# Optimization experiments

Hardware: AMD Instinct MI355X
Metric: run time of the kernel (lower is better)

The kernel has to match this reference:

```python
import jax, jax.numpy as jnp
import numpy as np

N = 50000      # nodes per graph side
E = 800000     # edges per graph side
G = 128        # number of graphs in the batch
D = 256        # input feature dim
L = 1024       # number of output labels
NEG_SLOPE = 0.2


def _gat_layer(x, src, dst, W, a_src, a_dst, b, n_nodes):
    """Single-head GATConv with self-loops already included in (src, dst)."""
    h = x @ W                                   # [N, F]
    s_src = h @ a_src                           # [N] per-node source score
    s_dst = h @ a_dst                           # [N] per-node dest score
    e = jax.nn.leaky_relu(s_src[src] + s_dst[dst], NEG_SLOPE)   # [E']
    m = jax.ops.segment_max(e, dst, num_segments=n_nodes)        # segment softmax (stable)
    ex = jnp.exp(e - m[dst])
    denom = jax.ops.segment_sum(ex, dst, num_segments=n_nodes)
    alpha = ex / denom[dst]                     # [E']
    out = jax.ops.segment_sum(h[src] * alpha[:, None], dst, num_segments=n_nodes)
    return out + b


def _mean_pool(x, batch, n_graphs):
    s = jax.ops.segment_sum(x, batch, num_segments=n_graphs)
    cnt = jax.ops.segment_sum(jnp.ones((x.shape[0],), x.dtype), batch, num_segments=n_graphs)
    return s / jnp.maximum(cnt, 1.0)[:, None]


def setup_inputs() -> dict:
    key = jax.random.key(0)
    ks = jax.random.split(key, 24)
    p = lambda k, shape: (jax.random.normal(k, shape, jnp.float32) * 0.05)
    inp = {
        "x_s": jax.random.normal(ks[0], (N, D), jnp.float32),
        "x_t": jax.random.normal(ks[1], (N, D), jnp.float32),
        "edge_index_s": jax.random.randint(ks[2], (2, E), 0, N, jnp.int32),
        "edge_index_t": jax.random.randint(ks[3], (2, E), 0, N, jnp.int32),
        "xs_batch": jnp.sort(jax.random.randint(ks[4], (N,), 0, G, jnp.int32)),
        "xt_batch": jnp.sort(jax.random.randint(ks[5], (N,), 0, G, jnp.int32)),
        # source-graph GAT layers: 256->128, 128->64
        "Ws1": p(ks[6], (D, D // 2)), "as1_src": p(ks[7], (D // 2,)), "as1_dst": p(ks[8], (D // 2,)), "bs1": jnp.zeros((D // 2,), jnp.float32),
        "Ws2": p(ks[9], (D // 2, D // 4)), "as2_src": p(ks[10], (D // 4,)), "as2_dst": p(ks[11], (D // 4,)), "bs2": jnp.zeros((D // 4,), jnp.float32),
        # target-graph GAT layers
        "Wt1": p(ks[12], (D, D // 2)), "at1_src": p(ks[13], (D // 2,)), "at1_dst": p(ks[14], (D // 2,)), "bt1": jnp.zeros((D // 2,), jnp.float32),
        "Wt2": p(ks[15], (D // 2, D // 4)), "at2_src": p(ks[16], (D // 4,)), "at2_dst": p(ks[17], (D // 4,)), "bt2": jnp.zeros((D // 4,), jnp.float32),
        # classifier head
        "Wlin": p(ks[18], (D // 4, L)), "blin": jnp.zeros((L,), jnp.float32),
    }
    return inp


def reference(x_s, x_t, edge_index_s, edge_index_t, xs_batch, xt_batch,
              Ws1, as1_src, as1_dst, bs1, Ws2, as2_src, as2_dst, bs2,
              Wt1, at1_src, at1_dst, bt1, Wt2, at2_src, at2_dst, bt2,
              Wlin, blin):
    loop = jnp.arange(N, dtype=edge_index_s.dtype)
    src_s = jnp.concatenate([edge_index_s[0], loop])   # add self-loops (PyG default)
    dst_s = jnp.concatenate([edge_index_s[1], loop])
    src_t = jnp.concatenate([edge_index_t[0], loop])
    dst_t = jnp.concatenate([edge_index_t[1], loop])

    x1 = jax.nn.relu(_gat_layer(x_s, src_s, dst_s, Ws1, as1_src, as1_dst, bs1, N))
    x2 = jax.nn.relu(_gat_layer(x1, src_s, dst_s, Ws2, as2_src, as2_dst, bs2, N))
    xs = _mean_pool(x2, xs_batch, G)                   # [G, 64]

    x3 = jax.nn.relu(_gat_layer(x_t, src_t, dst_t, Wt1, at1_src, at1_dst, bt1, N))
    x4 = jax.nn.relu(_gat_layer(x3, src_t, dst_t, Wt2, at2_src, at2_dst, bt2, N))
    xt = _mean_pool(x4, xt_batch, G)                   # [G, 64]

    out = (xs + xt) @ Wlin + blin                      # [G, L]
    return jax.nn.sigmoid(out)
```

## Files before the change

kernel.cpp:

```cpp
#include <hip/hip_runtime.h>
#include <hip/hip_bf16.h>
#include <math.h>

constexpr int Nn   = 50000;
constexpr int Ecnt = 800000;
constexpr int Gn   = 128;
constexpr int Din  = 256;
constexpr int Lout = 1024;

constexpr int BKT_SH = 7;
constexpr int NBKT   = (Nn + 127) >> BKT_SH;
constexpr int CHUNK  = 4096;
constexpr int EBC    = (Ecnt + CHUNK - 1) / CHUNK;
constexpr size_t HS  = (size_t)Nn * 64;

typedef __attribute__((ext_vector_type(8))) short short8;
typedef __attribute__((ext_vector_type(4))) float f32x4;
typedef __attribute__((ext_vector_type(2))) float v2f;

__device__ __forceinline__ float lrelu(float x) { return x >= 0.f ? x : 0.2f * x; }

__device__ __forceinline__ float bflo(uint32_t v) { return __uint_as_float(v << 16); }
__device__ __forceinline__ float bfhi(uint32_t v) { return __uint_as_float(v & 0xffff0000u); }
__device__ __forceinline__ uint32_t f2bf(float f) {
    uint32_t x = __float_as_uint(f);
    return (x + 0x7fffu + ((x >> 16) & 1u)) >> 16;
}
__device__ __forceinline__ uint32_t packbf(float lo, float hi) {
    return f2bf(lo) | (f2bf(hi) << 16);
}

__global__ __launch_bounds__(512) void bkt_scan2(const int* __restrict__ bkt_cnt_b,
                                                 int* __restrict__ bkt_ptr_b,
                                                 int* __restrict__ bkt_cur_b,
                                                 int* __restrict__ row_ptr_b) {
    int side = blockIdx.x;
    const int* bkt_cnt = bkt_cnt_b + (size_t)side * (NBKT + 1);
    int* bkt_ptr = bkt_ptr_b + (size_t)side * (NBKT + 1);
    int* bkt_cur = bkt_cur_b + (size_t)side * (NBKT + 1);
    int* row_ptr = row_ptr_b + (size_t)side * (Nn + 1);
    __shared__ int buf[512];
    int t = threadIdx.x;
    int v = (t < NBKT) ? bkt_cnt[t] : 0;
    buf[t] = v;
    __syncthreads();
    for (int off = 1; off < 512; off <<= 1) {
        int x = (t >= off) ? buf[t - off] : 0;
        __syncthreads();
        buf[t] += x;
        __syncthreads();
    }
    if (t < NBKT) {
        int excl = buf[t] - v;
        bkt_ptr[t] = excl;
        bkt_cur[t] = excl;
    }
    if (t == 511) {
        bkt_ptr[NBKT] = buf[511];
        row_ptr[Nn]   = buf[511];
    }
}

__global__ __launch_bounds__(256) void bkt_scatter2(const int* __restrict__ e0,
                                                    const int* __restrict__ e1,
                                                    int* __restrict__ bkt_cur_b,
                                                    uint32_t* __restrict__ bkt_edges_b, int E) {
    int side = blockIdx.y;
    const int* src = side ? e1 : e0;
    const int* dst = src + E;
    int* bkt_cur = bkt_cur_b + (size_t)side * (NBKT + 1);
    uint32_t* bkt_edges = bkt_edges_b + (size_t)side * Ecnt;
    __shared__ int h[NBKT];
    __shared__ int cur[NBKT];
    for (int i = threadIdx.x; i < NBKT; i += 256) h[i] = 0;
    __syncthreads();
    int base = blockIdx.x * CHUNK;
    int end = min(base + CHUNK, E);
    for (int i = base + threadIdx.x; i < end; i += 256)
        atomicAdd(&h[dst[i] >> BKT_SH], 1);
    __syncthreads();
    for (int i = threadIdx.x; i < NBKT; i += 256) {
        int c = h[i];
        h[i] = c ? atomicAdd(&bkt_cur[i], c) : 0;
        cur[i] = 0;
    }
    __syncthreads();
    for (int i = base + threadIdx.x; i < end; i += 256) {
        int d = dst[i], b = d >> BKT_SH;
        int pos = h[b] + atomicAdd(&cur[b], 1);
        bkt_edges[pos] = (uint32_t)src[i] | ((uint32_t)(d & 127) << 16);
    }
}

__global__ __launch_bounds__(256) void csr_finalize2(const uint32_t* __restrict__ bkt_edges_b,
                                                     const int* __restrict__ bkt_ptr_b,
                                                     int* __restrict__ row_ptr_b,
                                                     int* __restrict__ csr_b, int n) {
    int side = blockIdx.y;
    const uint32_t* bkt_edges = bkt_edges_b + (size_t)side * Ecnt;
    const int* bkt_ptr = bkt_ptr_b + (size_t)side * (NBKT + 1);
    int* row_ptr = row_ptr_b + (size_t)side * (Nn + 1);
    int* csr = csr_b + (size_t)side * Ecnt;
    int b = blockIdx.x;
    int base = bkt_ptr[b];
    int cnt  = bkt_ptr[b + 1] - base;
    __shared__ int hist[128], curs[128], sc[128];
    int t = threadIdx.x;
    if (t < 128) hist[t] = 0;
    __syncthreads();
    for (int i = t; i < cnt; i += 256)
        atomicAdd(&hist[(bkt_edges[base + i] >> 16) & 127], 1);
    __syncthreads();
    if (t < 128) sc[t] = hist[t];
    __syncthreads();
    for (int off = 1; off < 128; off <<= 1) {
        int x = (t >= off && t < 128) ? sc[t - off] : 0;
        __syncthreads();
        if (t < 128) sc[t] += x;
        __syncthreads();
    }
    if (t < 128) {
        int excl = sc[t] - hist[t];
        int node = (b << BKT_SH) + t;
        if (node < n) row_ptr[node] = base + excl;
        curs[t] = excl;
    }
    __syncthreads();
    for (int i = t; i < cnt; i += 256) {
        uint32_t e = bkt_edges[base + i];
        int pos = atomicAdd(&curs[(e >> 16) & 127], 1);
        csr[base + pos] = (int)(e & 0xFFFFu);
    }
}

template<int MF, int NF, int BN, bool BF16A, bool FUSE_COUNT>
__global__ __launch_bounds__(256) void mfma_gemm2(
        const void* __restrict__ A0, const void* __restrict__ A1,
        const float* __restrict__ B0, const float* __restrict__ B1,
        uint32_t* __restrict__ Cb, size_t cstride,
        const float* __restrict__ as0, const float* __restrict__ as1,
        const float* __restrict__ ad0, const float* __restrict__ ad1,
        float* __restrict__ ssrc_b, float* __restrict__ sdst_b,
        int M, int K,
        const int* __restrict__ e0, const int* __restrict__ e1,
        int* __restrict__ bkt_cnt_b) {
    __shared__ uint32_t Al[64][36];
    __shared__ uint32_t Bl[BN][36];
    __shared__ float sS[64][2], sD[64][2];
    int side = blockIdx.y;

    if constexpr (FUSE_COUNT) {
        int gb = (M + 63) >> 6;
        if ((int)blockIdx.x >= gb) {
            int chunk = blockIdx.x - gb;
            const int* dst = (side ? e1 : e0) + Ecnt;
            int* bkt_cnt = bkt_cnt_b + (size_t)side * (NBKT + 1);
            int* hh = (int*)&Al[0][0];
            for (int i = threadIdx.x; i < NBKT; i += 256) hh[i] = 0;
            __syncthreads();
            int base = chunk * CHUNK;
            int end = min(base + CHUNK, Ecnt);
            for (int i = base + threadIdx.x; i < end; i += 256)
                atomicAdd(&hh[dst[i] >> BKT_SH], 1);
            __syncthreads();
            for (int i = threadIdx.x; i < NBKT; i += 256) {
                int c = hh[i];
                if (c) atomicAdd(&bkt_cnt[i], c);
            }
            return;
        }
    }

    const void* Av = side ? A1 : A0;
    const float* B = side ? B1 : B0;
    const float* Asrc = side ? as1 : as0;
    const float* Adst = side ? ad1 : ad0;
    uint32_t* C = Cb + (size_t)side * cstride;
    float* ssrc = ssrc_b + (size_t)side * Nn;
    float* sdst = sdst_b + (size_t)side * Nn;

    int tid  = threadIdx.x;
    int lane = tid & 63;
    int wid  = tid >> 6;
    int wr = wid >> 1, wc = wid & 1;
    int bm = blockIdx.x * 64;

    int arow = tid >> 2, aq = tid & 3;
    bool avalid = (bm + arow) < M;
    constexpr int NPI = BN * 16 / 256;

    float    fA[16];
    uint32_t uA[8];
    float    fB[NPI][4];

    auto LOADA = [&](int k0) {
        if constexpr (BF16A) {
            const uint32_t* A = (const uint32_t*)Av;
            if (avalid) {
                const uint32_t* p = A + (size_t)(bm + arow) * (K >> 1) + (k0 >> 1) + aq * 8;
                uint4 u0 = *(const uint4*)p;
                uint4 u1 = *(const uint4*)(p + 4);
                uA[0] = u0.x; uA[1] = u0.y; uA[2] = u0.z; uA[3] = u0.w;
                uA[4] = u1.x; uA[5] = u1.y; uA[6] = u1.z; uA[7] = u1.w;
            } else {
                #pragma unroll
                for (int i = 0; i < 8; i++) uA[i] = 0u;
            }
        } else {
            const float* A = (const float*)Av;
            if (avalid) {
                const float* p = A + (size_t)(bm + arow) * K + k0 + aq * 16;
                #pragma unroll
                for (int i = 0; i < 4; i++) {
                    float4 f = *(const float4*)(p + i * 4);
                    fA[4 * i] = f.x; fA[4 * i + 1] = f.y; fA[4 * i + 2] = f.z; fA[4 * i + 3] = f.w;
                }
            } else {
                #pragma unroll
                for (int i = 0; i < 16; i++) fA[i] = 0.f;
            }
        }
    };
    auto LOADB = [&](int k0) {
        #pragma unroll
        for (int it = 0; it < NPI; it++) {
            int pi = tid + it * 256;
            int n = pi & (BN - 1);
            int kp = pi / BN;
            const float* p = B + (size_t)(k0 + 4 * kp) * BN + n;
            fB[it][0] = p[0];
            fB[it][1] = p[BN];
            fB[it][2] = p[2 * BN];
            fB[it][3] = p[3 * BN];
        }
    };
    auto WRITE = [&]() {
        if constexpr (BF16A) {
            uint4* dst = (uint4*)&Al[arow][aq * 8];
            dst[0] = make_uint4(uA[0], uA[1], uA[2], uA[3]);
            dst[1] = make_uint4(uA[4], uA[5], uA[6], uA[7]);
        } else {
            uint32_t d[8];
            #pragma unroll
            for (int i = 0; i < 8; i++) d[i] = packbf(fA[2 * i], fA[2 * i + 1]);
            uint4* dst = (uint4*)&Al[arow][aq * 8];
            dst[0] = make_uint4(d[0], d[1], d[2], d[3]);
            dst[1] = make_uint4(d[4], d[5], d[6], d[7]);
        }
        #pragma unroll
        for (int it = 0; it < NPI; it++) {
            int pi = tid + it * 256;
            int n = pi & (BN - 1);
            int kp = pi / BN;
            *(uint2*)&Bl[n][2 * kp] = make_uint2(packbf(fB[it][0], fB[it][1]),
                                                 packbf(fB[it][2], fB[it][3]));
        }
    };

    f32x4 acc[MF][NF];
    #pragma unroll
    for (int i = 0; i < MF; i++)
        #pragma unroll
        for (int j = 0; j < NF; j++) acc[i][j] = (f32x4){0.f, 0.f, 0.f, 0.f};

    LOADA(0); LOADB(0);
    const int T = K / 64;
    for (int t = 0; t < T; t++) {
        WRITE();
        __syncthreads();
        if (t + 1 < T) { LOADA((t + 1) * 64); LOADB((t + 1) * 64); }
        int lr = lane & 15, lk = lane >> 4;
        #pragma unroll
        for (int ks = 0; ks < 2; ks++) {
            short8 af[MF], bf[NF];
            #pragma unroll
            for (int mf = 0; mf < MF; mf++)
                af[mf] = *(const short8*)&Al[wr * (MF * 16) + mf * 16 + lr][ks * 16 + lk * 4];
            #pragma unroll
            for (int nf = 0; nf < NF; nf++)
                bf[nf] = *(const short8*)&Bl[wc * (NF * 16) + nf * 16 + lr][ks * 16 + lk * 4];
            #pragma unroll
            for (int mf = 0; mf < MF; mf++)
                #pragma unroll
                for (int nf = 0; nf < NF; nf++)
                    acc[mf][nf] = __builtin_amdgcn_mfma_f32_16x16x32_bf16(af[mf], bf[nf], acc[mf][nf], 0, 0, 0);
        }
        __syncthreads();
    }

    int lr = lane & 15, lg = lane >> 4;
    {
        float a_s[NF], a_d[NF];
        #pragma unroll
        for (int nf = 0; nf < NF; nf++) {
            int col = wc * (NF * 16) + nf * 16 + lr;
            a_s[nf] = Asrc[col];
            a_d[nf] = Adst[col];
        }
        #pragma unroll
        for (int mf = 0; mf < MF; mf++) {
            #pragma unroll
            for (int j = 0; j < 4; j++) {
                float ps = 0.f, pd = 0.f;
                #pragma unroll
                for (int nf = 0; nf < NF; nf++) {
                    float v = acc[mf][nf][j];
                    ps += v * a_s[nf];
                    pd += v * a_d[nf];
                }
                #pragma unroll
                for (int o = 1; o < 16; o <<= 1) {
                    ps += __shfl_xor(ps, o);
                    pd += __shfl_xor(pd, o);
                }
                if (lr == 0) {
                    int rl = wr * (MF * 16) + mf * 16 + lg * 4 + j;
                    sS[rl][wc] = ps;
                    sD[rl][wc] = pd;
                }
            }
        }
    }
    #pragma unroll
    for (int mf = 0; mf < MF; mf++) {
        #pragma unroll
        for (int nf = 0; nf < NF; nf++) {
            int col = wc * (NF * 16) + nf * 16 + lr;
            #pragma unroll
            for (int j = 0; j < 4; j++) {
                int row = bm + wr * (MF * 16) + mf * 16 + lg * 4 + j;
                float v = acc[mf][nf][j];
                float w1 = __shfl_xor(v, 1);
                uint32_t p01 = (uint32_t)__builtin_amdgcn_cvt_pk_fp8_f32(v, w1, 0, false);
                uint32_t p23 = __shfl_xor(p01, 2);
                if (((lane & 3) == 0) && row < M)
                    C[(size_t)row * (BN >> 2) + (col >> 2)] = (p01 & 0xffffu) | (p23 << 16);
            }
        }
    }
    __syncthreads();
    if (tid < 64) {
        int row = bm + tid;
        if (row < M) {
            ssrc[row] = sS[tid][0] + sS[tid][1];
            sdst[row] = sD[tid][0] + sD[tid][1];
        }
    }
}

template<int F>
__global__ __launch_bounds__(256) void attn_agg2(const uint32_t* __restrict__ hb,
        const float* __restrict__ ssrc_b, const float* __restrict__ sdst_b,
        const int* __restrict__ row_ptr_b, const int* __restrict__ csr_b,
        const float* __restrict__ bias0, const float* __restrict__ bias1,
        uint32_t* __restrict__ xout_b, int n) {
    constexpr size_t HSTR = (size_t)Nn * (F / 4);
    constexpr int HD = F / 4;
    constexpr int XD = F / 2;
    int side = blockIdx.y;
    const uint32_t* h = hb + (size_t)side * HSTR;
    const float* ssrc = ssrc_b + (size_t)side * Nn;
    const float* sdst = sdst_b + (size_t)side * Nn;
    const int* row_ptr = row_ptr_b + (size_t)side * (Nn + 1);
    const int* csr_src = csr_b + (size_t)side * Ecnt;
    const float* bias = side ? bias1 : bias0;
    uint32_t* xout = xout_b + (size_t)side * HS;

    int wave = (blockIdx.x * blockDim.x + threadIdx.x) >> 6;
    int lane = threadIdx.x & 63;
    int half = lane >> 5;
    int lane5 = lane & 31;
    int wid = wave * 2 + half;
    if (wid >= n) return;
    int beg = row_ptr[wid], end = row_ptr[wid + 1];
    int deg = end - beg;
    float sd = sdst[wid];
    float eself = lrelu(ssrc[wid] + sd);
    int base32 = lane & 32;

    v2f a0 = {0.f, 0.f}, a1 = {0.f, 0.f}, a2 = {0.f, 0.f}, a3 = {0.f, 0.f};
    auto FMA8 = [&](uint2 u, float wj) {
        v2f p0 = __builtin_amdgcn_cvt_pk_f32_fp8(u.x, false);
        v2f p1 = __builtin_amdgcn_cvt_pk_f32_fp8(u.x, true);
        v2f p2 = __builtin_amdgcn_cvt_pk_f32_fp8(u.y, false);
        v2f p3 = __builtin_amdgcn_cvt_pk_f32_fp8(u.y, true);
        v2f wv = {wj, wj};
        a0 += p0 * wv; a1 += p1 * wv; a2 += p2 * wv; a3 += p3 * wv;
    };

    if (deg <= 32) {
        int p = beg + lane5;
        bool act = lane5 < deg;
        int s = act ? csr_src[p] : 0;
        float e = act ? lrelu(ssrc[s] + sd) : -1e30f;
        float m = fmaxf(eself, e);
        #pragma unroll
        for (int o = 16; o; o >>= 1) m = fmaxf(m, __shfl_xor(m, o));
        float ex = act ? __expf(e - m) : 0.f;
        float dsum = ex;
        #pragma unroll
        for (int o = 16; o; o >>= 1) dsum += __shfl_xor(dsum, o);
        float exself = __expf(eself - m);
        dsum += exself;
        float inv = 1.f / dsum;
        float w = ex * inv;
        float wself = exself * inv;

        if constexpr (F == 128) {
            int slot = (lane >> 4) & 1, i = lane & 15;
            size_t foff = 2 * i;
            if (slot == 0) FMA8(*(const uint2*)(h + (size_t)wid * HD + foff), wself);
            int j = slot;
            for (; j + 6 < deg; j += 8) {
                float w0 = __shfl(w, base32 | j),       w1 = __shfl(w, base32 | (j + 2));
                float w2 = __shfl(w, base32 | (j + 4)), w3 = __shfl(w, base32 | (j + 6));
                int   s0 = __shfl(s, base32 | j),       s1 = __shfl(s, base32 | (j + 2));
                int   s2 = __shfl(s, base32 | (j + 4)), s3 = __shfl(s, base32 | (j + 6));
                uint2 u0 = *(const uint2*)(h + (size_t)s0 * HD + foff);
                uint2 u1 = *(const uint2*)(h + (size_t)s1 * HD + foff);
                uint2 u2 = *(const uint2*)(h + (size_t)s2 * HD + foff);
                uint2 u3 = *(const uint2*)(h + (size_t)s3 * HD + foff);
                FMA8(u0, w0); FMA8(u1, w1); FMA8(u2, w2); FMA8(u3, w3);
            }
            for (; j < deg; j += 2) {
                float w0 = __shfl(w, base32 | j);
                int   s0 = __shfl(s, base32 | j);
                FMA8(*(const uint2*)(h + (size_t)s0 * HD + foff), w0);
            }
            a0[0] += __shfl_xor(a0[0], 16); a0[1] += __shfl_xor(a0[1], 16);
            a1[0] += __shfl_xor(a1[0], 16); a1[1] += __shfl_xor(a1[1], 16);
            a2[0] += __shfl_xor(a2[0], 16); a2[1] += __shfl_xor(a2[1], 16);
            a3[0] += __shfl_xor(a3[0], 16); a3[1] += __shfl_xor(a3[1], 16);
            if (!(lane & 16)) {
                float r0 = fmaxf(a0[0] + bias[8*i],   0.f), r1 = fmaxf(a0[1] + bias[8*i+1], 0.f);
                float r2 = fmaxf(a1[0] + bias[8*i+2], 0.f), r3 = fmaxf(a1[1] + bias[8*i+3], 0.f);
                float r4 = fmaxf(a2[0] + bias[8*i+4], 0.f), r5 = fmaxf(a2[1] + bias[8*i+5], 0.f);
                float r6 = fmaxf(a3[0] + bias[8*i+6], 0.f), r7 = fmaxf(a3[1] + bias[8*i+7], 0.f);
                *(uint4*)(xout + (size_t)wid * XD + 4 * i) =
                    make_uint4(packbf(r0, r1), packbf(r2, r3), packbf(r4, r5), packbf(r6, r7));
            }
        } else {
            int g = (lane >> 3) & 3, i = lane & 7;
            size_t foff = 2 * i;
            if (g == 0) FMA8(*(const uint2*)(h + (size_t)wid * HD + foff), wself);
            int j = g;
            for (; j + 12 < deg; j += 16) {
                float w0 = __shfl(w, base32 | j),       w1 = __shfl(w, base32 | (j + 4));
                float w2 = __shfl(w, base32 | (j + 8)), w3 = __shfl(w, base32 | (j + 12));
                int   s0 = __shfl(s, base32 | j),       s1 = __shfl(s, base32 | (j + 4));
                int   s2 = __shfl(s, base32 | (j + 8)), s3 = __shfl(s, base32 | (j + 12));
                uint2 u0 = *(const uint2*)(h + (size_t)s0 * HD + foff);
                uint2 u1 = *(const uint2*)(h + (size_t)s1 * HD + foff);
                uint2 u2 = *(const uint2*)(h + (size_t)s2 * HD + foff);
                uint2 u3 = *(const uint2*)(h + (size_t)s3 * HD + foff);
                FMA8(u0, w0); FMA8(u1, w1); FMA8(u2, w2); FMA8(u3, w3);
            }
            for (; j < deg; j += 4) {
                float w0 = __shfl(w, base32 | j);
                int   s0 = __shfl(s, base32 | j);
                FMA8(*(const uint2*)(h + (size_t)s0 * HD + foff), w0);
            }
            #pragma unroll
            for (int o = 8; o <= 16; o <<= 1) {
                a0[0] += __shfl_xor(a0[0], o); a0[1] += __shfl_xor(a0[1], o);
                a1[0] += __shfl_xor(a1[0], o); a1[1] += __shfl_xor(a1[1], o);
                a2[0] += __shfl_xor(a2[0], o); a2[1] += __shfl_xor(a2[1], o);
                a3[0] += __shfl_xor(a3[0], o); a3[1] += __shfl_xor(a3[1], o);
            }
            if (!(lane & 24)) {
                float r0 = fmaxf(a0[0] + bias[8*i],   0.f), r1 = fmaxf(a0[1] + bias[8*i+1], 0.f);
                float r2 = fmaxf(a1[0] + bias[8*i+2], 0.f), r3 = fmaxf(a1[1] + bias[8*i+3], 0.f);
                float r4 = fmaxf(a2[0] + bias[8*i+4], 0.f), r5 = fmaxf(a2[1] + bias[8*i+5], 0.f);
                float r6 = fmaxf(a3[0] + bias[8*i+6], 0.f), r7 = fmaxf(a3[1] + bias[8*i+7], 0.f);
                *(uint4*)(xout + (size_t)wid * XD + 4 * i) =
                    make_uint4(packbf(r0, r1), packbf(r2, r3), packbf(r4, r5), packbf(r6, r7));
            }
        }
        return;
    }

    float m = eself;
    for (int p = beg + lane5; p < end; p += 32)
        m = fmaxf(m, lrelu(ssrc[csr_src[p]] + sd));
    #pragma unroll
    for (int o = 16; o; o >>= 1) m = fmaxf(m, __shfl_xor(m, o));
    float dsum = (lane5 == 0) ? __expf(eself - m) : 0.f;
    for (int p = beg + lane5; p < end; p += 32)
        dsum += __expf(lrelu(ssrc[csr_src[p]] + sd) - m);
    #pragma unroll
    for (int o = 16; o; o >>= 1) dsum += __shfl_xor(dsum, o);
    float inv = 1.f / dsum;
    float wself = __expf(eself - m) * inv;

    if constexpr (F == 128) {
        int slot = (lane >> 4) & 1, i = lane & 15;
        size_t foff = 2 * i;
        if (slot == 0) FMA8(*(const uint2*)(h + (size_t)wid * HD + foff), wself);
        for (int j = slot; j < deg; j += 2) {
            int sj = csr_src[beg + j];
            float wj = __expf(lrelu(ssrc[sj] + sd) - m) * inv;
            FMA8(*(const uint2*)(h + (size_t)sj * HD + foff), wj);
        }
        a0[0] += __shfl_xor(a0[0], 16); a0[1] += __shfl_xor(a0[1], 16);
        a1[0] += __shfl_xor(a1[0], 16); a1[1] += __shfl_xor(a1[1], 16);
        a2[0] += __shfl_xor(a2[0], 16); a2[1] += __shfl_xor(a2[1], 16);
        a3[0] += __shfl_xor(a3[0], 16); a3[1] += __shfl_xor(a3[1], 16);
        if (!(lane & 16)) {
            float r0 = fmaxf(a0[0] + bias[8*i],   0.f), r1 = fmaxf(a0[1] + bias[8*i+1], 0.f);
            float r2 = fmaxf(a1[0] + bias[8*i+2], 0.f), r3 = fmaxf(a1[1] + bias[8*i+3], 0.f);
            float r4 = fmaxf(a2[0] + bias[8*i+4], 0.f), r5 = fmaxf(a2[1] + bias[8*i+5], 0.f);
            float r6 = fmaxf(a3[0] + bias[8*i+6], 0.f), r7 = fmaxf(a3[1] + bias[8*i+7], 0.f);
            *(uint4*)(xout + (size_t)wid * XD + 4 * i) =
                make_uint4(packbf(r0, r1), packbf(r2, r3), packbf(r4, r5), packbf(r6, r7));
        }
    } else {
        int g = (lane >> 3) & 3, i = lane & 7;
        size_t foff = 2 * i;
        if (g == 0) FMA8(*(const uint2*)(h + (size_t)wid * HD + foff), wself);
        for (int j = g; j < deg; j += 4) {
            int sj = csr_src[beg + j];
            float wj = __expf(lrelu(ssrc[sj] + sd) - m) * inv;
            FMA8(*(const uint2*)(h + (size_t)sj * HD + foff), wj);
        }
        #pragma unroll
        for (int o = 8; o <= 16; o <<= 1) {
            a0[0] += __shfl_xor(a0[0], o); a0[1] += __shfl_xor(a0[1], o);
            a1[0] += __shfl_xor(a1[0], o); a1[1] += __shfl_xor(a1[1], o);
            a2[0] += __shfl_xor(a2[0], o); a2[1] += __shfl_xor(a2[1], o);
            a3[0] += __shfl_xor(a3[0], o); a3[1] += __shfl_xor(a3[1], o);
        }
        if (!(lane & 24)) {
            float r0 = fmaxf(a0[0] + bias[8*i],   0.f), r1 = fmaxf(a0[1] + bias[8*i+1], 0.f);
            float r2 = fmaxf(a1[0] + bias[8*i+2], 0.f), r3 = fmaxf(a1[1] + bias[8*i+3], 0.f);
            float r4 = fmaxf(a2[0] + bias[8*i+4], 0.f), r5 = fmaxf(a2[1] + bias[8*i+5], 0.f);
            float r6 = fmaxf(a3[0] + bias[8*i+6], 0.f), r7 = fmaxf(a3[1] + bias[8*i+7], 0.f);
            *(uint4*)(xout + (size_t)wid * XD + 4 * i) =
                make_uint4(packbf(r0, r1), packbf(r2, r3), packbf(r4, r5), packbf(r6, r7));
        }
    }
}

__global__ __launch_bounds__(256) void pool2(const uint32_t* __restrict__ xb,
                                             const int* __restrict__ bat0,
                                             const int* __restrict__ bat1,
                                             float* __restrict__ pooled_b, int n) {
    int side = blockIdx.y;
    const uint32_t* x = xb + (size_t)side * HS;
    const int* batch = side ? bat1 : bat0;
    float* pooled = pooled_b + (size_t)side * Gn * 64;
    int g = blockIdx.x;
    int tid = threadIdx.x;
    __shared__ int s_lo, s_hi;
    if (tid == 0) {
        int lo = 0, hi = n;
        while (lo < hi) { int mid = (lo + hi) >> 1; if (batch[mid] < g) lo = mid + 1; else hi = mid; }
        s_lo = lo;
        int lo2 = lo, hi2 = n;
        while (lo2 < hi2) { int mid = (lo2 + hi2) >> 1; if (batch[mid] < g + 1) lo2 = mid + 1; else hi2 = mid; }
        s_hi = lo2;
    }
    __syncthreads();
    int lo = s_lo, hi = s_hi;
    int grp = tid >> 5, col = tid & 31;
    float a0 = 0.f, a1 = 0.f;
    for (int i = lo + grp; i < hi; i += 8) {
        uint32_t v = x[(size_t)i * 32 + col];
        a0 += bflo(v);
        a1 += bfhi(v);
    }
    __shared__ float red0[8][32], red1[8][32];
    red0[grp][col] = a0;
    red1[grp][col] = a1;
    __syncthreads();
    if (tid < 32) {
        float s0 = 0.f, s1 = 0.f;
        #pragma unroll
        for (int r = 0; r < 8; r++) { s0 += red0[r][tid]; s1 += red1[r][tid]; }
        float c = fmaxf((float)(hi - lo), 1.f);
        pooled[g * 64 + 2 * tid]     = s0 / c;
        pooled[g * 64 + 2 * tid + 1] = s1 / c;
    }
}

__global__ __launch_bounds__(256) void head_kernel(const float* __restrict__ xs,
                                                   const float* __restrict__ xt,
                                                   const float* __restrict__ Wlin,
                                                   const float* __restrict__ blin,
                                                   float* __restrict__ out) {
    int g = blockIdx.y;
    int c = blockIdx.x * 256 + threadIdx.x;
    __shared__ float z[64];
    if (threadIdx.x < 64) z[threadIdx.x] = xs[g * 64 + threadIdx.x] + xt[g * 64 + threadIdx.x];
    __syncthreads();
    float a0 = 0.f, a1 = 0.f, a2 = 0.f, a3 = 0.f;
    #pragma unroll
    for (int k = 0; k < 64; k += 4) {
        a0 += z[k]     * Wlin[(size_t)(k)     * Lout + c];
        a1 += z[k + 1] * Wlin[(size_t)(k + 1) * Lout + c];
        a2 += z[k + 2] * Wlin[(size_t)(k + 2) * Lout + c];
        a3 += z[k + 3] * Wlin[(size_t)(k + 3) * Lout + c];
    }
    float acc = (a0 + a1) + (a2 + a3) + blin[c];
    out[(size_t)g * Lout + c] = 1.f / (1.f + expf(-acc));
}

extern "C" void kernel_launch(void* const* d_in, const int* in_sizes, int n_in,
                              void* d_out, int out_size, void* d_ws, size_t ws_size,
                              hipStream_t stream) {
    size_t off = 0;
    auto alloc = [&](size_t bytes) -> void* {
        void* p = (char*)d_ws + off;
        off += (bytes + 255) & ~(size_t)255;
        return p;
    };
    uint32_t* hbuf    = (uint32_t*)alloc(2 * (size_t)Nn * 32 * 4);
    uint32_t* xbuf    = (uint32_t*)alloc(2 * HS * 4);
    float* ssrc       = (float*)alloc(2 * (size_t)Nn * 4);
    float* sdst       = (float*)alloc(2 * (size_t)Nn * 4);
    int*   row_ptr    = (int*)alloc(2 * (size_t)(Nn + 1) * 4);
    int*   csr        = (int*)alloc(2 * (size_t)Ecnt * 4);
    uint32_t* bkt_edges = (uint32_t*)alloc(2 * (size_t)Ecnt * 4);
    int*   bkt_cnt    = (int*)alloc(2 * (size_t)(NBKT + 1) * 4);
    int*   bkt_ptr    = (int*)alloc(2 * (size_t)(NBKT + 1) * 4);
    int*   bkt_cur    = (int*)alloc(2 * (size_t)(NBKT + 1) * 4);
    float* pooled     = (float*)alloc(2 * (size_t)Gn * 64 * 4);

    const int NW2 = (((Nn + 1) / 2) * 64 + 255) / 256;
    const int GB  = (Nn + 63) / 64;

    const float* x_s = (const float*)d_in[0];
    const float* x_t = (const float*)d_in[1];
    const int* ei_s  = (const int*)d_in[2];
    const int* ei_t  = (const int*)d_in[3];
    const int* bat_s = (const int*)d_in[4];
    const int* bat_t = (const int*)d_in[5];
    const float *Ws1 = (const float*)d_in[6],  *as1s = (const float*)d_in[7],
                *as1d = (const float*)d_in[8],  *bs1 = (const float*)d_in[9];
    const float *Ws2 = (const float*)d_in[10], *as2s = (const float*)d_in[11],
                *as2d = (const float*)d_in[12], *bs2 = (const float*)d_in[13];
    const float *Wt1 = (const float*)d_in[14], *at1s = (const float*)d_in[15],
                *at1d = (const float*)d_in[16], *bt1 = (const float*)d_in[17];
    const float *Wt2 = (const float*)d_in[18], *at2s = (const float*)d_in[19],
                *at2d = (const float*)d_in[20], *bt2 = (const float*)d_in[21];
    const float *Wlin = (const float*)d_in[22], *blin = (const float*)d_in[23];

    hipMemsetAsync(bkt_cnt, 0, 2 * (size_t)(NBKT + 1) * 4, stream);
    mfma_gemm2<2, 4, 128, false, true><<<dim3(GB + EBC, 2), 256, 0, stream>>>(
        x_s, x_t, Ws1, Wt1, hbuf, (size_t)Nn * 32, as1s, at1s, as1d, at1d, ssrc, sdst, Nn, Din,
        ei_s, ei_t, bkt_cnt);
    bkt_scan2<<<2, 512, 0, stream>>>(bkt_cnt, bkt_ptr, bkt_cur, row_ptr);
    bkt_scatter2<<<dim3(EBC, 2), 256, 0, stream>>>(ei_s, ei_t, bkt_cur, bkt_edges, Ecnt);
    csr_finalize2<<<dim3(NBKT, 2), 256, 0, stream>>>(bkt_edges, bkt_ptr, row_ptr, csr, Nn);
    attn_agg2<128><<<dim3(NW2, 2), 256, 0, stream>>>(hbuf, ssrc, sdst, row_ptr, csr, bs1, bt1, xbuf, Nn);
    mfma_gemm2<2, 2, 64, true, false><<<dim3(GB, 2), 256, 0, stream>>>(
        xbuf, xbuf + HS, Ws2, Wt2, hbuf, (size_t)Nn * 16, as2s, at2s, as2d, at2d, ssrc, sdst, Nn, 128,
        nullptr, nullptr, nullptr);
    attn_agg2<64><<<dim3(NW2, 2), 256, 0, stream>>>(hbuf, ssrc, sdst, row_ptr, csr, bs2, bt2, xbuf, Nn);
    pool2<<<dim3(Gn, 2), 256, 0, stream>>>(xbuf, bat_s, bat_t, pooled, Nn);
    head_kernel<<<dim3(Lout / 256, Gn), 256, 0, stream>>>(pooled, pooled + (size_t)Gn * 64,
                                                          Wlin, blin, (float*)d_out);
}
```

Measured before the change: 207.6 us.

## Keep full weight matrix in LDS and stream A fragments directly into registers

The GEMM kernel now loads the entire bf16-packed weight matrix (all of K) into shared memory once per block and has each wave load its A-row fragments straight from global memory into registers, double-buffered across k-steps, instead of staging A and B tiles through LDS every 64-wide K step. Each wave now owns the full N width, so the per-row attention score partials are written directly without a shared-memory reduction, and the block covers 128 rows instead of 64. This removes the per-iteration barriers and LDS traffic for A. In exchange it uses larger LDS allocations, more registers and uncoalesced per-lane row reads of A, and launches half as many GEMM blocks.

```diff
diff --git a/kernel.cpp b/kernel.cpp
--- a/kernel.cpp
+++ b/kernel.cpp
@@ -133,7 +133,7 @@
     }
 }
 
-template<int MF, int NF, int BN, bool BF16A, bool FUSE_COUNT>
+template<int MF, int NF, int KT, bool BF16A, bool FUSE_COUNT>
 __global__ __launch_bounds__(256) void mfma_gemm2(
         const void* __restrict__ A0, const void* __restrict__ A1,
         const float* __restrict__ B0, const float* __restrict__ B1,
@@ -141,21 +141,25 @@
         const float* __restrict__ as0, const float* __restrict__ as1,
         const float* __restrict__ ad0, const float* __restrict__ ad1,
         float* __restrict__ ssrc_b, float* __restrict__ sdst_b,
-        int M, int K,
+        int M,
         const int* __restrict__ e0, const int* __restrict__ e1,
         int* __restrict__ bkt_cnt_b) {
-    __shared__ uint32_t Al[64][36];
-    __shared__ uint32_t Bl[BN][36];
-    __shared__ float sS[64][2], sD[64][2];
+    constexpr int BM  = 4 * MF * 16;
+    constexpr int BN  = NF * 16;
+    constexpr int KD  = KT / 2;
+    constexpr int LDB = KD + 4;
+    constexpr int S   = KT / 32;
+    constexpr int BSH = (BN == 128) ? 7 : 6;
+    __shared__ uint32_t Bl[BN][LDB];
     int side = blockIdx.y;
 
     if constexpr (FUSE_COUNT) {
-        int gb = (M + 63) >> 6;
+        int gb = (M + BM - 1) / BM;
         if ((int)blockIdx.x >= gb) {
             int chunk = blockIdx.x - gb;
             const int* dst = (side ? e1 : e0) + Ecnt;
             int* bkt_cnt = bkt_cnt_b + (size_t)side * (NBKT + 1);
-            int* hh = (int*)&Al[0][0];
+            int* hh = (int*)&Bl[0][0];
             for (int i = threadIdx.x; i < NBKT; i += 256) hh[i] = 0;
             __syncthreads();
             int base = chunk * CHUNK;
@@ -182,80 +186,29 @@
     int tid  = threadIdx.x;
     int lane = tid & 63;
     int wid  = tid >> 6;
-    int wr = wid >> 1, wc = wid & 1;
-    int bm = blockIdx.x * 64;
-
-    int arow = tid >> 2, aq = tid & 3;
-    bool avalid = (bm + arow) < M;
-    constexpr int NPI = BN * 16 / 256;
-
-    float    fA[16];
-    uint32_t uA[8];
-    float    fB[NPI][4];
-
-    auto LOADA = [&](int k0) {
-        if constexpr (BF16A) {
-            const uint32_t* A = (const uint32_t*)Av;
-            if (avalid) {
-                const uint32_t* p = A + (size_t)(bm + arow) * (K >> 1) + (k0 >> 1) + aq * 8;
-                uint4 u0 = *(const uint4*)p;
-                uint4 u1 = *(const uint4*)(p + 4);
-                uA[0] = u0.x; uA[1] = u0.y; uA[2] = u0.z; uA[3] = u0.w;
-                uA[4] = u1.x; uA[5] = u1.y; uA[6] = u1.z; uA[7] = u1.w;
-            } else {
-                #pragma unroll
-                for (int i = 0; i < 8; i++) uA[i] = 0u;
-            }
-        } else {
-            const float* A = (const float*)Av;
-            if (avalid) {
-                const float* p = A + (size_t)(bm + arow) * K + k0 + aq * 16;
-                #pragma unroll
-                for (int i = 0; i < 4; i++) {
-                    float4 f = *(const float4*)(p + i * 4);
-                    fA[4 * i] = f.x; fA[4 * i + 1] = f.y; fA[4 * i + 2] = f.z; fA[4 * i + 3] = f.w;
-                }
-            } else {
-                #pragma unroll
-                for (int i = 0; i < 16; i++) fA[i] = 0.f;
-            }
-        }
-    };
-    auto LOADB = [&](int k0) {
-        #pragma unroll
-        for (int it = 0; it < NPI; it++) {
-            int pi = tid + it * 256;
-            int n = pi & (BN - 1);
-            int kp = pi / BN;
-            const float* p = B + (size_t)(k0 + 4 * kp) * BN + n;
-            fB[it][0] = p[0];
-            fB[it][1] = p[BN];
-            fB[it][2] = p[2 * BN];
-            fB[it][3] = p[3 * BN];
-        }
-    };
-    auto WRITE = [&]() {
-        if constexpr (BF16A) {
-            uint4* dst = (uint4*)&Al[arow][aq * 8];
-            dst[0] = make_uint4(uA[0], uA[1], uA[2], uA[3]);
-            dst[1] = make_uint4(uA[4], uA[5], uA[6], uA[7]);
-        } else {
-            uint32_t d[8];
-            #pragma unroll
-            for (int i = 0; i < 8; i++) d[i] = packbf(fA[2 * i], fA[2 * i + 1]);
-            uint4* dst = (uint4*)&Al[arow][aq * 8];
-            dst[0] = make_uint4(d[0], d[1], d[2], d[3]);
-            dst[1] = make_uint4(d[4], d[5], d[6], d[7]);
-        }
-        #pragma unroll
-        for (int it = 0; it < NPI; it++) {
-            int pi = tid + it * 256;
-            int n = pi & (BN - 1);
-            int kp = pi / BN;
-            *(uint2*)&Bl[n][2 * kp] = make_uint2(packbf(fB[it][0], fB[it][1]),
-                                                 packbf(fB[it][2], fB[it][3]));
-        }
-    };
+    int bm = blockIdx.x * BM;
+
+    for (int idx = tid; idx < BN * KD; idx += 256) {
+        int n  = idx & (BN - 1);
+        int kd = idx >> BSH;
+        float b0 = B[(size_t)(2 * kd) * BN + n];
+        float b1 = B[(size_t)(2 * kd + 1) * BN + n];
+        Bl[n][kd] = packbf(b0, b1);
+    }
+    __syncthreads();
+
+    int lr = lane & 15, lk = lane >> 4;
+    int wrow = bm + wid * (MF * 16);
+
+    const float*    ArF[MF];
+    const uint32_t* ArU[MF];
+    #pragma unroll
+    for (int mf = 0; mf < MF; mf++) {
+        int r = wrow + mf * 16 + lr;
+        r = r < M ? r : (M - 1);
+        if constexpr (BF16A) ArU[mf] = (const uint32_t*)Av + (size_t)r * KD;
+        else                 ArF[mf] = (const float*)Av + (size_t)r * KT;
+    }
 
     f32x4 acc[MF][NF];
     #pragma unroll
@@ -263,39 +216,59 @@
         #pragma unroll
         for (int j = 0; j < NF; j++) acc[i][j] = (f32x4){0.f, 0.f, 0.f, 0.f};
 
-    LOADA(0); LOADB(0);
-    const int T = K / 64;
-    for (int t = 0; t < T; t++) {
-        WRITE();
-        __syncthreads();
-        if (t + 1 < T) { LOADA((t + 1) * 64); LOADB((t + 1) * 64); }
-        int lr = lane & 15, lk = lane >> 4;
-        #pragma unroll
-        for (int ks = 0; ks < 2; ks++) {
-            short8 af[MF], bf[NF];
-            #pragma unroll
-            for (int mf = 0; mf < MF; mf++)
-                af[mf] = *(const short8*)&Al[wr * (MF * 16) + mf * 16 + lr][ks * 16 + lk * 4];
+    uint4  ru[2][MF];
+    float4 rf0[2][MF], rf1[2][MF];
+
+    auto LOADRAW = [&](int ks, int b) {
+        #pragma unroll
+        for (int mf = 0; mf < MF; mf++) {
+            if constexpr (BF16A) {
+                ru[b][mf] = *(const uint4*)(ArU[mf] + ks * 16 + lk * 4);
+            } else {
+                const float* p = ArF[mf] + ks * 32 + lk * 8;
+                rf0[b][mf] = *(const float4*)p;
+                rf1[b][mf] = *(const float4*)(p + 4);
+            }
+        }
+    };
+
+    LOADRAW(0, 0);
+    #pragma unroll
+    for (int ks = 0; ks < S; ks++) {
+        if (ks + 1 < S) LOADRAW(ks + 1, (ks + 1) & 1);
+        short8 af[MF];
+        #pragma unroll
+        for (int mf = 0; mf < MF; mf++) {
+            if constexpr (BF16A) {
+                af[mf] = __builtin_bit_cast(short8, ru[ks & 1][mf]);
+            } else {
+                float4 f0 = rf0[ks & 1][mf], f1 = rf1[ks & 1][mf];
+                uint4 t;
+                t.x = packbf(f0.x, f0.y);
+                t.y = packbf(f0.z, f0.w);
+                t.z = packbf(f1.x, f1.y);
+                t.w = packbf(f1.z, f1.w);
+                af[mf] = __builtin_bit_cast(short8, t);
+            }
+        }
+        short8 bf[NF];
+        #pragma unroll
+        for (int nf = 0; nf < NF; nf++)
+            bf[nf] = *(const short8*)&Bl[nf * 16 + lr][ks * 16 + lk * 4];
+        #pragma unroll
+        for (int mf = 0; mf < MF; mf++)
             #pragma unroll
             for (int nf = 0; nf < NF; nf++)
-                bf[nf] = *(const short8*)&Bl[wc * (NF * 16) + nf * 16 + lr][ks * 16 + lk * 4];
-            #pragma unroll
-            for (int mf = 0; mf < MF; mf++)
-                #pragma unroll
-                for (int nf = 0; nf < NF; nf++)
-                    acc[mf][nf] = __builtin_amdgcn_mfma_f32_16x16x32_bf16(af[mf], bf[nf], acc[mf][nf], 0, 0, 0);
-        }
-        __syncthreads();
-    }
-
-    int lr = lane & 15, lg = lane >> 4;
+                acc[mf][nf] = __builtin_amdgcn_mfma_f32_16x16x32_bf16(af[mf], bf[nf], acc[mf][nf], 0, 0, 0);
+    }
+
+    int lg = lane >> 4;
     {
         float a_s[NF], a_d[NF];
         #pragma unroll
         for (int nf = 0; nf < NF; nf++) {
-            int col = wc * (NF * 16) + nf * 16 + lr;
-            a_s[nf] = Asrc[col];
-            a_d[nf] = Adst[col];
+            a_s[nf] = Asrc[nf * 16 + lr];
+            a_d[nf] = Adst[nf * 16 + lr];
         }
         #pragma unroll
         for (int mf = 0; mf < MF; mf++) {
@@ -313,10 +286,10 @@
                     ps += __shfl_xor(ps, o);
                     pd += __shfl_xor(pd, o);
                 }
-                if (lr == 0) {
-                    int rl = wr * (MF * 16) + mf * 16 + lg * 4 + j;
-                    sS[rl][wc] = ps;
-                    sD[rl][wc] = pd;
+                int row = wrow + mf * 16 + lg * 4 + j;
+                if (lr == 0 && row < M) {
+                    ssrc[row] = ps;
+                    sdst[row] = pd;
                 }
             }
         }
@@ -325,10 +298,10 @@
     for (int mf = 0; mf < MF; mf++) {
         #pragma unroll
         for (int nf = 0; nf < NF; nf++) {
-            int col = wc * (NF * 16) + nf * 16 + lr;
+            int col = nf * 16 + lr;
             #pragma unroll
             for (int j = 0; j < 4; j++) {
-                int row = bm + wr * (MF * 16) + mf * 16 + lg * 4 + j;
+                int row = wrow + mf * 16 + lg * 4 + j;
                 float v = acc[mf][nf][j];
                 float w1 = __shfl_xor(v, 1);
                 uint32_t p01 = (uint32_t)__builtin_amdgcn_cvt_pk_fp8_f32(v, w1, 0, false);
@@ -336,14 +309,6 @@
                 if (((lane & 3) == 0) && row < M)
                     C[(size_t)row * (BN >> 2) + (col >> 2)] = (p01 & 0xffffu) | (p23 << 16);
             }
-        }
-    }
-    __syncthreads();
-    if (tid < 64) {
-        int row = bm + tid;
-        if (row < M) {
-            ssrc[row] = sS[tid][0] + sS[tid][1];
-            sdst[row] = sD[tid][0] + sD[tid][1];
         }
     }
 }
@@ -626,7 +591,7 @@
     float* pooled     = (float*)alloc(2 * (size_t)Gn * 64 * 4);
 
     const int NW2 = (((Nn + 1) / 2) * 64 + 255) / 256;
-    const int GB  = (Nn + 63) / 64;
+    const int GB  = (Nn + 127) / 128;
 
     const float* x_s = (const float*)d_in[0];
     const float* x_t = (const float*)d_in[1];
@@ -645,15 +610,15 @@
     const float *Wlin = (const float*)d_in[22], *blin = (const float*)d_in[23];
 
     hipMemsetAsync(bkt_cnt, 0, 2 * (size_t)(NBKT + 1) * 4, stream);
-    mfma_gemm2<2, 4, 128, false, true><<<dim3(GB + EBC, 2), 256, 0, stream>>>(
-        x_s, x_t, Ws1, Wt1, hbuf, (size_t)Nn * 32, as1s, at1s, as1d, at1d, ssrc, sdst, Nn, Din,
+    mfma_gemm2<2, 8, 256, false, true><<<dim3(GB + EBC, 2), 256, 0, stream>>>(
+        x_s, x_t, Ws1, Wt1, hbuf, (size_t)Nn * 32, as1s, at1s, as1d, at1d, ssrc, sdst, Nn,
         ei_s, ei_t, bkt_cnt);
     bkt_scan2<<<2, 512, 0, stream>>>(bkt_cnt, bkt_ptr, bkt_cur, row_ptr);
     bkt_scatter2<<<dim3(EBC, 2), 256, 0, stream>>>(ei_s, ei_t, bkt_cur, bkt_edges, Ecnt);
     csr_finalize2<<<dim3(NBKT, 2), 256, 0, stream>>>(bkt_edges, bkt_ptr, row_ptr, csr, Nn);
     attn_agg2<128><<<dim3(NW2, 2), 256, 0, stream>>>(hbuf, ssrc, sdst, row_ptr, csr, bs1, bt1, xbuf, Nn);
-    mfma_gemm2<2, 2, 64, true, false><<<dim3(GB, 2), 256, 0, stream>>>(
-        xbuf, xbuf + HS, Ws2, Wt2, hbuf, (size_t)Nn * 16, as2s, at2s, as2d, at2d, ssrc, sdst, Nn, 128,
+    mfma_gemm2<2, 4, 128, true, false><<<dim3(GB, 2), 256, 0, stream>>>(
+        xbuf, xbuf + HS, Ws2, Wt2, hbuf, (size_t)Nn * 16, as2s, at2s, as2d, at2d, ssrc, sdst, Nn,
         nullptr, nullptr, nullptr);
     attn_agg2<64><<<dim3(NW2, 2), 256, 0, stream>>>(hbuf, ssrc, sdst, row_ptr, csr, bs2, bt2, xbuf, Nn);
     pool2<<<dim3(Gn, 2), 256, 0, stream>>>(xbuf, bat_s, bat_t, pooled, Nn);
```

Result: no change. 211.5 us (+1.8%).
